# Optimization experiments

Measured on AMD Instinct MI355X. Metric: run time of the kernel, lower is better.

Reference implementation:

```python
import jax, jax.numpy as jnp
import numpy as np

EMBED_DIM = 400
NUM_HEADS = 4
HEAD_SIZE = EMBED_DIM // NUM_HEADS  # 100


def setup_inputs() -> dict:
    key = jax.random.key(0)
    ks = jax.random.split(key, 6)
    B, T = 8, 2048
    x = jax.random.normal(ks[0], (B, T, EMBED_DIM), dtype=jnp.float32)
    # per-head projection weights, stacked over heads: [H, C, D]
    scale = 1.0 / np.sqrt(EMBED_DIM)
    Wq = jax.random.normal(ks[1], (NUM_HEADS, EMBED_DIM, HEAD_SIZE), dtype=jnp.float32) * scale
    Wk = jax.random.normal(ks[2], (NUM_HEADS, EMBED_DIM, HEAD_SIZE), dtype=jnp.float32) * scale
    Wv = jax.random.normal(ks[3], (NUM_HEADS, EMBED_DIM, HEAD_SIZE), dtype=jnp.float32) * scale
    Wo = jax.random.normal(ks[4], (EMBED_DIM, EMBED_DIM), dtype=jnp.float32) * scale
    bo = jax.random.normal(ks[5], (EMBED_DIM,), dtype=jnp.float32) * scale
    return {"x": x, "Wq": Wq, "Wk": Wk, "Wv": Wv, "Wo": Wo, "bo": bo}


def reference(x, Wq, Wk, Wv, Wo, bo):
    B, T, C = x.shape
    inv_sqrt_d = 1.0 / jnp.sqrt(jnp.asarray(HEAD_SIZE, x.dtype))
    # project: [B,T,C] x [H,C,D] -> [B,H,T,D]
    q = jnp.einsum('btc,hcd->bhtd', x, Wq)
    k = jnp.einsum('btc,hcd->bhtd', x, Wk)
    v = jnp.einsum('btc,hcd->bhtd', x, Wv)
    scores = jnp.einsum('bhtd,bhsd->bhts', q, k) * inv_sqrt_d  # [B,H,T,T]
    causal = jnp.tril(jnp.ones((T, T), dtype=bool))
    scores = jnp.where(causal, scores, -jnp.inf)
    attn = jax.nn.softmax(scores, axis=-1)
    out = jnp.einsum('bhts,bhsd->bhtd', attn, v)  # [B,H,T,D]
    # concat heads (head order matches torch concat on last dim)
    out = out.transpose(0, 2, 1, 3).reshape(B, T, C)
    # output projection; dropout is identity in eval mode
    return out @ Wo.T + bo
```

## Files before the change

kernel.cpp:

```cpp
#include <hip/hip_runtime.h>
#include <hip/hip_bf16.h>

#define B_ 8
#define T_ 2048
#define C_ 400
#define H_ 4
#define D_ 100
#define DP 128
#define KP 416
#define KPB 832

typedef __hip_bfloat16 bf16;
typedef unsigned int uint32;
typedef __attribute__((ext_vector_type(8))) short short8;
typedef __attribute__((ext_vector_type(4))) float f32x4;

__device__ __forceinline__ float bf2f(bf16 v){ return __bfloat162float(v); }
__device__ __forceinline__ bf16 f2bf(float f){ return __float2bfloat16(f); }
__device__ __forceinline__ unsigned short bfbits(float f){
  bf16 h = f2bf(f);
  return __builtin_bit_cast(unsigned short, h);
}
__device__ __forceinline__ uint32 pk2(float a, float b){
  return (uint32)bfbits(a) | ((uint32)bfbits(b) << 16);
}
__device__ __forceinline__ void gl_lds16(const char* gsrc, char* ldst){
  __builtin_amdgcn_global_load_lds(
      (const __attribute__((address_space(1))) unsigned int*)gsrc,
      (__attribute__((address_space(3))) unsigned int*)ldst, 16, 0, 0);
}

__global__ __launch_bounds__(256) void conv_x_kernel(const float* __restrict__ x,
    bf16* __restrict__ xb){
  int i = blockIdx.x*256 + threadIdx.x;
  if (i >= 16384*52) return;
  int c8 = i % 52, t = i / 52;
  uint32 u[4];
  if (c8 < 50){
    const float* src = x + (size_t)t*C_ + c8*8;
    #pragma unroll
    for (int k=0;k<4;++k) u[k] = pk2(src[2*k], src[2*k+1]);
  } else {
    u[0]=u[1]=u[2]=u[3]=0;
  }
  *reinterpret_cast<uint4*>((char*)xb + (size_t)t*KPB + c8*16) = make_uint4(u[0],u[1],u[2],u[3]);
}

__global__ __launch_bounds__(256) void prep_wqkv_kernel(const float* __restrict__ Wq,
    const float* __restrict__ Wk, const float* __restrict__ Wv, bf16* __restrict__ WT){
  int i = blockIdx.x*256 + threadIdx.x;
  if (i >= 12*128*KP) return;
  int c = i % KP, n = (i/KP) & 127, group = i/(KP*128);
  int p = group >> 2, h = group & 3;
  float v = 0.f;
  if (n < D_ && c < C_){
    const float* W = (p==0)?Wq:(p==1)?Wk:Wv;
    v = W[((size_t)h*C_ + c)*D_ + n];
  }
  WT[i] = f2bf(v);
}

__global__ __launch_bounds__(256) void prep_wo_kernel(const float* __restrict__ Wo,
    bf16* __restrict__ WoB){
  int i = blockIdx.x*256 + threadIdx.x;
  if (i >= 512*KP) return;
  int c = i % KP, n = i / KP;
  float v = (n < C_ && c < C_) ? Wo[(size_t)n*C_ + c] : 0.f;
  WoB[i] = f2bf(v);
}

__global__ __launch_bounds__(256) void zero_aopad_kernel(bf16* __restrict__ AOb){
  int i = blockIdx.x*256 + threadIdx.x;
  if (i >= 16384*2) return;
  int row = i >> 1, half = i & 1;
  *reinterpret_cast<uint4*>((char*)AOb + (size_t)row*KPB + 800 + half*16) = make_uint4(0,0,0,0);
}

__global__ __launch_bounds__(256) void qkv_gemm_kernel(const bf16* __restrict__ xb,
    const bf16* __restrict__ WT, bf16* __restrict__ Qp, bf16* __restrict__ Kp,
    bf16* __restrict__ VT){
  __shared__ __align__(16) char xs[2][8192];
  __shared__ __align__(16) char wsh[2][8192];
  int bid = blockIdx.x;
  int xcd = bid & 7, idx = bid >> 3;
  int mb = xcd*16 + idx/12;
  int group = idx % 12;
  int p = group >> 2, h = group & 3;
  int t0 = mb * 128;
  int tid = threadIdx.x;
  int w = tid >> 6, l = tid & 63, g = l >> 4, qi = l & 15;
  const char* xg = (const char*)xb + (size_t)t0*KPB;
  const char* wg = (const char*)WT + (size_t)group*128*KPB;
  int srow = tid >> 2, sseg = tid & 3;

  #define GSTAGE(J, BUF) {                                                     \
    int kc2 = (J)*64;                                                          \
    _Pragma("unroll")                                                          \
    for (int r2=0;r2<2;++r2)                                                   \
      gl_lds16(xg + (size_t)(srow + r2*64)*KPB + kc2 + sseg*16,                \
               &xs[BUF][tid*16 + r2*4096]);                                    \
    _Pragma("unroll")                                                          \
    for (int r2=0;r2<2;++r2)                                                   \
      gl_lds16(wg + (size_t)(srow + r2*64)*KPB + kc2 + sseg*16,                \
               &wsh[BUF][tid*16 + r2*4096]); }

  f32x4 acc[2][8];
  #pragma unroll
  for (int mt=0;mt<2;++mt)
    #pragma unroll
    for (int nt=0;nt<8;++nt) acc[mt][nt] = (f32x4){0.f,0.f,0.f,0.f};

  GSTAGE(0, 0)
  __syncthreads();
  for (int j = 0; j < 13; ++j){
    int cur = j & 1;
    if (j < 12) GSTAGE(j+1, cur^1)
    short8 af[2];
    #pragma unroll
    for (int mt=0;mt<2;++mt)
      af[mt] = *reinterpret_cast<const short8*>(&xs[cur][(w*32 + mt*16 + qi)*64 + g*16]);
    short8 bfr[8];
    #pragma unroll
    for (int nt=0;nt<8;++nt)
      bfr[nt] = *reinterpret_cast<const short8*>(&wsh[cur][(nt*16 + qi)*64 + g*16]);
    if (p < 2){
      #pragma unroll
      for (int mt=0;mt<2;++mt)
        #pragma unroll
        for (int nt=0;nt<8;++nt)
          acc[mt][nt] = __builtin_amdgcn_mfma_f32_16x16x32_bf16(af[mt], bfr[nt], acc[mt][nt], 0,0,0);
    } else {
      #pragma unroll
      for (int mt=0;mt<2;++mt)
        #pragma unroll
        for (int nt=0;nt<8;++nt)
          acc[mt][nt] = __builtin_amdgcn_mfma_f32_16x16x32_bf16(bfr[nt], af[mt], acc[mt][nt], 0,0,0);
    }
    __syncthreads();
  }

  int b = t0 >> 11, tloc0 = t0 & 2047;
  size_t bh = (size_t)b*H_ + h;
  if (p < 2){
    bf16* dst = (p==0 ? Qp : Kp) + (bh*T_ + tloc0)*DP;
    #pragma unroll
    for (int mt=0;mt<2;++mt)
      #pragma unroll
      for (int r=0;r<4;++r){
        int tr = w*32 + mt*16 + 4*g + r;
        #pragma unroll
        for (int nt=0;nt<8;++nt)
          dst[(size_t)tr*DP + nt*16 + qi] = f2bf(acc[mt][nt][r]);
      }
  } else {
    bf16* dstv = VT + bh*DP*T_ + tloc0;
    #pragma unroll
    for (int nt=0;nt<8;++nt)
      #pragma unroll
      for (int r=0;r<4;++r){
        int d = nt*16 + 4*g + r;
        #pragma unroll
        for (int mt=0;mt<2;++mt)
          dstv[(size_t)d*T_ + w*32 + mt*16 + qi] = f2bf(acc[mt][nt][r]);
      }
  }
  #undef GSTAGE
}

__global__ __launch_bounds__(256) void out_gemm_kernel(const bf16* __restrict__ AOb,
    const bf16* __restrict__ WoB, const float* __restrict__ bo, float* __restrict__ out){
  __shared__ __align__(16) char xs[2][8192];
  __shared__ __align__(16) char wsh[2][8192];
  int bid = blockIdx.x;
  int xcd = bid & 7, idx = bid >> 3;
  int mb = xcd*16 + idx/4;
  int nb = idx & 3;
  int t0 = mb * 128, n0 = nb * 128;
  int tid = threadIdx.x;
  int w = tid >> 6, l = tid & 63, g = l >> 4, qi = l & 15;
  const char* xg = (const char*)AOb + (size_t)t0*KPB;
  const char* wg = (const char*)WoB + (size_t)n0*KPB;
  int srow = tid >> 2, sseg = tid & 3;

  #define GSTAGE(J, BUF) {                                                     \
    int kc2 = (J)*64;                                                          \
    _Pragma("unroll")                                                          \
    for (int r2=0;r2<2;++r2)                                                   \
      gl_lds16(xg + (size_t)(srow + r2*64)*KPB + kc2 + sseg*16,                \
               &xs[BUF][tid*16 + r2*4096]);                                    \
    _Pragma("unroll")                                                          \
    for (int r2=0;r2<2;++r2)                                                   \
      gl_lds16(wg + (size_t)(srow + r2*64)*KPB + kc2 + sseg*16,                \
               &wsh[BUF][tid*16 + r2*4096]); }

  f32x4 acc[2][8];
  #pragma unroll
  for (int mt=0;mt<2;++mt)
    #pragma unroll
    for (int nt=0;nt<8;++nt) acc[mt][nt] = (f32x4){0.f,0.f,0.f,0.f};

  GSTAGE(0, 0)
  __syncthreads();
  for (int j = 0; j < 13; ++j){
    int cur = j & 1;
    if (j < 12) GSTAGE(j+1, cur^1)
    short8 af[2];
    #pragma unroll
    for (int mt=0;mt<2;++mt)
      af[mt] = *reinterpret_cast<const short8*>(&xs[cur][(w*32 + mt*16 + qi)*64 + g*16]);
    short8 bfr[8];
    #pragma unroll
    for (int nt=0;nt<8;++nt)
      bfr[nt] = *reinterpret_cast<const short8*>(&wsh[cur][(nt*16 + qi)*64 + g*16]);
    #pragma unroll
    for (int mt=0;mt<2;++mt)
      #pragma unroll
      for (int nt=0;nt<8;++nt)
        acc[mt][nt] = __builtin_amdgcn_mfma_f32_16x16x32_bf16(af[mt], bfr[nt], acc[mt][nt], 0,0,0);
    __syncthreads();
  }

  #pragma unroll
  for (int nt=0;nt<8;++nt){
    if (n0 + nt*16 >= C_) continue;
    int n = n0 + nt*16 + qi;
    float bv = bo[n];
    #pragma unroll
    for (int mt=0;mt<2;++mt)
      #pragma unroll
      for (int r=0;r<4;++r){
        int tr = w*32 + mt*16 + 4*g + r;
        out[(size_t)(t0 + tr)*C_ + n] = acc[mt][nt][r] + bv;
      }
  }
  #undef GSTAGE
}

__global__ __launch_bounds__(256) void attn_kernel(const bf16* __restrict__ Qp,
    const bf16* __restrict__ Kp, const bf16* __restrict__ VT, bf16* __restrict__ AOb){
  __shared__ __align__(16) char ktile[2][16384];
  __shared__ __align__(16) char vtile[2][14336];
  __shared__ __align__(16) uint32 pshare[4*16*36];
  const float NEGINF = -__builtin_inff();
  int bid = blockIdx.x;
  int xcd = bid & 7, idx = bid >> 3;
  int bh  = xcd*4 + (idx >> 5);
  int qb  = 31 - (idx & 31);
  int tid = threadIdx.x;
  int w = tid >> 6, l = tid & 63;
  int g = l >> 4, qi = l & 15;
  int q0 = qb*64 + w*16;

  const bf16* Qrow  = Qp + ((size_t)bh*T_ + q0 + qi)*DP + g*8;
  const char* Kg    = (const char*)(Kp + (size_t)bh*T_*DP);
  const char* Vg    = (const char*)(VT + (size_t)bh*DP*T_);

  short8 qf[4];
  #pragma unroll
  for (int ks=0; ks<4; ++ks)
    qf[ks] = *reinterpret_cast<const short8*>(Qrow + ks*32);

  f32x4 acc[7];
  #pragma unroll
  for (int dt=0; dt<7; ++dt) acc[dt] = (f32x4){0.f,0.f,0.f,0.f};
  float m = NEGINF, lr = 0.f;

  uint32* pbase = &pshare[(w*16 + qi)*36];
  int qglob = q0 + qi;
  int nch = qb + 1;

  int st_off0 = w*4096 + l*16;
  #define STAGE(J, BUF) { int k0s = (J) << 6;                                   \
    _Pragma("unroll")                                                           \
    for (int it=0; it<4; ++it){                                                 \
      int off = st_off0 + it*1024;                                              \
      int row = off >> 8;                                                       \
      int cb  = off & 255;                                                      \
      gl_lds16(Kg + (size_t)(k0s + row)*256 + (cb ^ ((row&15)<<4)),             \
               &ktile[BUF][w*4096 + it*1024]); } }

  #define VSTAGE(J, BUF) { int k0s2 = ((J) << 6)*2;                             \
    for (int it=w; it<14; it+=4){                                               \
      int off = it*1024 + l*16;                                                 \
      int row = off >> 7;                                                       \
      int cb  = off & 127;                                                      \
      gl_lds16(Vg + (size_t)row*(T_*2) + k0s2 + (cb ^ ((row&7)<<4)),            \
               &vtile[BUF][it*1024 + l*16]); } }

  STAGE(0, 0)
  VSTAGE(0, 0)
  __syncthreads();

  for (int j = 0; j < nch; ++j){
    int k0 = j << 6;
    int cur = j & 1;
    if (j + 1 < nch){ STAGE(j+1, cur^1) VSTAGE(j+1, cur^1) }
    const char* kb = ktile[cur];
    const char* vb = vtile[cur];
    f32x4 st[4];
    __builtin_amdgcn_s_setprio(1);
    #pragma unroll
    for (int kt=0; kt<4; ++kt){
      f32x4 s = (f32x4){0.f,0.f,0.f,0.f};
      #pragma unroll
      for (int ks=0; ks<4; ++ks){
        short8 kf = *reinterpret_cast<const short8*>(
            kb + (kt*16 + qi)*256 + ((ks*64 + g*16) ^ (qi<<4)));
        s = __builtin_amdgcn_mfma_f32_16x16x32_bf16(kf, qf[ks], s, 0, 0, 0);
      }
      st[kt] = s;
    }
    __builtin_amdgcn_s_setprio(0);
    float p[4][4];
    float cmax = NEGINF;
    if (j == nch - 1){
      #pragma unroll
      for (int kt=0; kt<4; ++kt)
        #pragma unroll
        for (int r=0; r<4; ++r){
          int key = k0 + kt*16 + 4*g + r;
          float v = st[kt][r]*0.1f; if (key > qglob) v = NEGINF;
          p[kt][r] = v; cmax = fmaxf(cmax, v);
        }
    } else {
      #pragma unroll
      for (int kt=0; kt<4; ++kt)
        #pragma unroll
        for (int r=0; r<4; ++r){
          float v = st[kt][r]*0.1f;
          p[kt][r] = v; cmax = fmaxf(cmax, v);
        }
    }
    cmax = fmaxf(cmax, __shfl_xor(cmax, 16));
    cmax = fmaxf(cmax, __shfl_xor(cmax, 32));
    float mnew = fmaxf(m, cmax);
    float scale = __expf(m - mnew);
    m = mnew;
    float rs = 0.f;
    #pragma unroll
    for (int kt=0; kt<4; ++kt)
      #pragma unroll
      for (int r=0; r<4; ++r){
        p[kt][r] = __expf(p[kt][r] - m);
        rs += p[kt][r];
      }
    rs += __shfl_xor(rs, 16);
    rs += __shfl_xor(rs, 32);
    lr = lr*scale + rs;
    float scr[4];
    #pragma unroll
    for (int r=0; r<4; ++r) scr[r] = __shfl(scale, 20*g + r);
    #pragma unroll
    for (int dt=0; dt<7; ++dt){
      acc[dt][0]*=scr[0]; acc[dt][1]*=scr[1]; acc[dt][2]*=scr[2]; acc[dt][3]*=scr[3];
    }
    #pragma unroll
    for (int kt=0; kt<4; ++kt){
      pbase[kt*8 + 2*g    ] = pk2(p[kt][0], p[kt][1]);
      pbase[kt*8 + 2*g + 1] = pk2(p[kt][2], p[kt][3]);
    }
    __builtin_amdgcn_s_setprio(1);
    #pragma unroll
    for (int ks=0; ks<2; ++ks){
      short8 pa = *reinterpret_cast<const short8*>(pbase + 16*ks + 4*g);
      #pragma unroll
      for (int dt=0; dt<7; ++dt){
        int row = dt*16 + qi;
        short8 vf = *reinterpret_cast<const short8*>(
            vb + row*128 + ((ks*64 + g*16) ^ ((qi&7)<<4)));
        acc[dt] = __builtin_amdgcn_mfma_f32_16x16x32_bf16(pa, vf, acc[dt], 0, 0, 0);
      }
    }
    __builtin_amdgcn_s_setprio(0);
    __syncthreads();
  }
  float inv = 1.f / lr;
  float invr[4];
  #pragma unroll
  for (int r=0; r<4; ++r) invr[r] = __shfl(inv, 20*g + r);
  int b = bh >> 2, h = bh & 3;
  #pragma unroll
  for (int dt=0; dt<7; ++dt){
    int d = dt*16 + qi;
    if (d < D_){
      #pragma unroll
      for (int r=0; r<4; ++r){
        size_t row = (size_t)(b*T_) + q0 + 4*g + r;
        AOb[row*KP + h*D_ + d] = f2bf(acc[dt][r] * invr[r]);
      }
    }
  }
  #undef STAGE
  #undef VSTAGE
}

extern "C" void kernel_launch(void* const* d_in, const int* in_sizes, int n_in,
                              void* d_out, int out_size, void* d_ws, size_t ws_size,
                              hipStream_t stream){
  const float* x  = (const float*)d_in[0];
  const float* Wq = (const float*)d_in[1];
  const float* Wk = (const float*)d_in[2];
  const float* Wv = (const float*)d_in[3];
  const float* Wo = (const float*)d_in[4];
  const float* bo = (const float*)d_in[5];

  constexpr size_t NBH  = (size_t)B_*H_;
  constexpr size_t NPAD = NBH*T_*DP;
  constexpr size_t NROW = (size_t)B_*T_;
  constexpr size_t OFF_QP  = 0;
  constexpr size_t OFF_KP  = OFF_QP + NPAD*2;
  constexpr size_t OFF_VT  = OFF_KP + NPAD*2;
  constexpr size_t OFF_XB  = OFF_VT + NPAD*2;
  constexpr size_t OFF_AOB = OFF_XB + NROW*KP*2;
  constexpr size_t OFF_WT  = OFF_AOB + NROW*KP*2;
  constexpr size_t OFF_WOB = OFF_WT + (size_t)12*128*KP*2;
  constexpr size_t TOTAL   = OFF_WOB + (size_t)512*KP*2;
  if (ws_size < TOTAL) return;

  char* ws = (char*)d_ws;
  bf16*  Qp   = (bf16*)(ws + OFF_QP);
  bf16*  Kp   = (bf16*)(ws + OFF_KP);
  bf16*  VTp  = (bf16*)(ws + OFF_VT);
  bf16*  xb   = (bf16*)(ws + OFF_XB);
  bf16*  AOb  = (bf16*)(ws + OFF_AOB);
  bf16*  WT   = (bf16*)(ws + OFF_WT);
  bf16*  WoB  = (bf16*)(ws + OFF_WOB);
  float* out  = (float*)d_out;

  conv_x_kernel<<<(16384*52 + 255)/256, 256, 0, stream>>>(x, xb);
  prep_wqkv_kernel<<<(12*128*KP + 255)/256, 256, 0, stream>>>(Wq, Wk, Wv, WT);
  prep_wo_kernel<<<(512*KP + 255)/256, 256, 0, stream>>>(Wo, WoB);
  zero_aopad_kernel<<<128, 256, 0, stream>>>(AOb);
  qkv_gemm_kernel<<<1536, 256, 0, stream>>>(xb, WT, Qp, Kp, VTp);
  attn_kernel<<<NBH*32, 256, 0, stream>>>(Qp, Kp, VTp, AOb);
  out_gemm_kernel<<<512, 256, 0, stream>>>(AOb, WoB, bo, out);
}
```

Baseline: 166.4 us.

## Double attention query tile per block, fold softmax scale into Q, lazy rescale

Each attention block now processes 128 queries (two 16-row query tiles per wave) instead of 64, so every staged K/V tile in LDS is reused across twice as many queries and the grid shrinks to 512 blocks. The 1/sqrt(d)*log2(e) factor is folded into Q at projection time so the softmax uses exp2 without a per-score multiply. Rescaling of the running output is skipped unless the row max grows by more than a threshold. Chunks lying entirely above the causal diagonal for a wave are skipped. The cost is more registers per thread (launch bounds set to 2 blocks), fewer blocks for load balancing across the causal triangle, and a small bf16 rounding change from scaling Q before conversion.

```diff
diff --git a/kernel.cpp b/kernel.cpp
--- a/kernel.cpp
+++ b/kernel.cpp
@@ -9,6 +9,7 @@
 #define DP 128
 #define KP 416
 #define KPB 832
+#define QSCALE 0.14426950408889634f
 
 typedef __hip_bfloat16 bf16;
 typedef unsigned int uint32;
@@ -142,6 +143,7 @@
   int b = t0 >> 11, tloc0 = t0 & 2047;
   size_t bh = (size_t)b*H_ + h;
   if (p < 2){
+    float qs = (p==0) ? QSCALE : 1.0f;
     bf16* dst = (p==0 ? Qp : Kp) + (bh*T_ + tloc0)*DP;
     #pragma unroll
     for (int mt=0;mt<2;++mt)
@@ -150,7 +152,7 @@
         int tr = w*32 + mt*16 + 4*g + r;
         #pragma unroll
         for (int nt=0;nt<8;++nt)
-          dst[(size_t)tr*DP + nt*16 + qi] = f2bf(acc[mt][nt][r]);
+          dst[(size_t)tr*DP + nt*16 + qi] = f2bf(qs * acc[mt][nt][r]);
       }
   } else {
     bf16* dstv = VT + bh*DP*T_ + tloc0;
@@ -236,38 +238,40 @@
   #undef GSTAGE
 }
 
-__global__ __launch_bounds__(256) void attn_kernel(const bf16* __restrict__ Qp,
+__global__ __launch_bounds__(256, 2) void attn_kernel(const bf16* __restrict__ Qp,
     const bf16* __restrict__ Kp, const bf16* __restrict__ VT, bf16* __restrict__ AOb){
   __shared__ __align__(16) char ktile[2][16384];
   __shared__ __align__(16) char vtile[2][14336];
-  __shared__ __align__(16) uint32 pshare[4*16*36];
+  __shared__ __align__(16) uint32 pshare[4*2*16*36];
   const float NEGINF = -__builtin_inff();
   int bid = blockIdx.x;
   int xcd = bid & 7, idx = bid >> 3;
-  int bh  = xcd*4 + (idx >> 5);
-  int qb  = 31 - (idx & 31);
+  int bh  = xcd*4 + (idx >> 4);
+  int qb  = 15 - (idx & 15);
   int tid = threadIdx.x;
   int w = tid >> 6, l = tid & 63;
   int g = l >> 4, qi = l & 15;
-  int q0 = qb*64 + w*16;
+  int q0 = qb*128 + w*32;
 
   const bf16* Qrow  = Qp + ((size_t)bh*T_ + q0 + qi)*DP + g*8;
   const char* Kg    = (const char*)(Kp + (size_t)bh*T_*DP);
   const char* Vg    = (const char*)(VT + (size_t)bh*DP*T_);
 
-  short8 qf[4];
-  #pragma unroll
-  for (int ks=0; ks<4; ++ks)
-    qf[ks] = *reinterpret_cast<const short8*>(Qrow + ks*32);
-
-  f32x4 acc[7];
-  #pragma unroll
-  for (int dt=0; dt<7; ++dt) acc[dt] = (f32x4){0.f,0.f,0.f,0.f};
-  float m = NEGINF, lr = 0.f;
-
-  uint32* pbase = &pshare[(w*16 + qi)*36];
-  int qglob = q0 + qi;
-  int nch = qb + 1;
+  short8 qf[2][4];
+  #pragma unroll
+  for (int qt=0; qt<2; ++qt)
+    #pragma unroll
+    for (int ks=0; ks<4; ++ks)
+      qf[qt][ks] = *reinterpret_cast<const short8*>(Qrow + qt*16*DP + ks*32);
+
+  f32x4 acc[2][7];
+  #pragma unroll
+  for (int qt=0; qt<2; ++qt)
+    #pragma unroll
+    for (int dt=0; dt<7; ++dt) acc[qt][dt] = (f32x4){0.f,0.f,0.f,0.f};
+  float m[2] = {NEGINF, NEGINF}, lr[2] = {0.f, 0.f};
+
+  int nch = 2*qb + 2;
 
   int st_off0 = w*4096 + l*16;
   #define STAGE(J, BUF) { int k0s = (J) << 6;                                   \
@@ -295,98 +299,113 @@
     int k0 = j << 6;
     int cur = j & 1;
     if (j + 1 < nch){ STAGE(j+1, cur^1) VSTAGE(j+1, cur^1) }
-    const char* kb = ktile[cur];
-    const char* vb = vtile[cur];
-    f32x4 st[4];
-    __builtin_amdgcn_s_setprio(1);
-    #pragma unroll
-    for (int kt=0; kt<4; ++kt){
-      f32x4 s = (f32x4){0.f,0.f,0.f,0.f};
-      #pragma unroll
-      for (int ks=0; ks<4; ++ks){
-        short8 kf = *reinterpret_cast<const short8*>(
-            kb + (kt*16 + qi)*256 + ((ks*64 + g*16) ^ (qi<<4)));
-        s = __builtin_amdgcn_mfma_f32_16x16x32_bf16(kf, qf[ks], s, 0, 0, 0);
-      }
-      st[kt] = s;
-    }
-    __builtin_amdgcn_s_setprio(0);
-    float p[4][4];
-    float cmax = NEGINF;
-    if (j == nch - 1){
-      #pragma unroll
-      for (int kt=0; kt<4; ++kt)
-        #pragma unroll
-        for (int r=0; r<4; ++r){
-          int key = k0 + kt*16 + 4*g + r;
-          float v = st[kt][r]*0.1f; if (key > qglob) v = NEGINF;
-          p[kt][r] = v; cmax = fmaxf(cmax, v);
-        }
-    } else {
-      #pragma unroll
-      for (int kt=0; kt<4; ++kt)
-        #pragma unroll
-        for (int r=0; r<4; ++r){
-          float v = st[kt][r]*0.1f;
-          p[kt][r] = v; cmax = fmaxf(cmax, v);
-        }
-    }
-    cmax = fmaxf(cmax, __shfl_xor(cmax, 16));
-    cmax = fmaxf(cmax, __shfl_xor(cmax, 32));
-    float mnew = fmaxf(m, cmax);
-    float scale = __expf(m - mnew);
-    m = mnew;
-    float rs = 0.f;
-    #pragma unroll
-    for (int kt=0; kt<4; ++kt)
-      #pragma unroll
-      for (int r=0; r<4; ++r){
-        p[kt][r] = __expf(p[kt][r] - m);
-        rs += p[kt][r];
-      }
-    rs += __shfl_xor(rs, 16);
-    rs += __shfl_xor(rs, 32);
-    lr = lr*scale + rs;
-    float scr[4];
-    #pragma unroll
-    for (int r=0; r<4; ++r) scr[r] = __shfl(scale, 20*g + r);
-    #pragma unroll
-    for (int dt=0; dt<7; ++dt){
-      acc[dt][0]*=scr[0]; acc[dt][1]*=scr[1]; acc[dt][2]*=scr[2]; acc[dt][3]*=scr[3];
-    }
-    #pragma unroll
-    for (int kt=0; kt<4; ++kt){
-      pbase[kt*8 + 2*g    ] = pk2(p[kt][0], p[kt][1]);
-      pbase[kt*8 + 2*g + 1] = pk2(p[kt][2], p[kt][3]);
-    }
-    __builtin_amdgcn_s_setprio(1);
-    #pragma unroll
-    for (int ks=0; ks<2; ++ks){
-      short8 pa = *reinterpret_cast<const short8*>(pbase + 16*ks + 4*g);
-      #pragma unroll
-      for (int dt=0; dt<7; ++dt){
-        int row = dt*16 + qi;
-        short8 vf = *reinterpret_cast<const short8*>(
-            vb + row*128 + ((ks*64 + g*16) ^ ((qi&7)<<4)));
-        acc[dt] = __builtin_amdgcn_mfma_f32_16x16x32_bf16(pa, vf, acc[dt], 0, 0, 0);
+    if (k0 <= q0 + 31){
+      const char* kb = ktile[cur];
+      const char* vb = vtile[cur];
+      bool lastm = (k0 + 63 > q0);
+      #pragma unroll
+      for (int qt=0; qt<2; ++qt){
+        int qglob = q0 + qt*16 + qi;
+        f32x4 st[4];
+        __builtin_amdgcn_s_setprio(1);
+        #pragma unroll
+        for (int kt=0; kt<4; ++kt){
+          f32x4 s = (f32x4){0.f,0.f,0.f,0.f};
+          #pragma unroll
+          for (int ks=0; ks<4; ++ks){
+            short8 kf = *reinterpret_cast<const short8*>(
+                kb + (kt*16 + qi)*256 + ((ks*64 + g*16) ^ (qi<<4)));
+            s = __builtin_amdgcn_mfma_f32_16x16x32_bf16(kf, qf[qt][ks], s, 0, 0, 0);
+          }
+          st[kt] = s;
+        }
+        __builtin_amdgcn_s_setprio(0);
+        float p[4][4];
+        float cmax = NEGINF;
+        if (lastm){
+          #pragma unroll
+          for (int kt=0; kt<4; ++kt)
+            #pragma unroll
+            for (int r=0; r<4; ++r){
+              int key = k0 + kt*16 + 4*g + r;
+              float v = st[kt][r]; if (key > qglob) v = NEGINF;
+              p[kt][r] = v; cmax = fmaxf(cmax, v);
+            }
+        } else {
+          #pragma unroll
+          for (int kt=0; kt<4; ++kt)
+            #pragma unroll
+            for (int r=0; r<4; ++r){
+              float v = st[kt][r];
+              p[kt][r] = v; cmax = fmaxf(cmax, v);
+            }
+        }
+        cmax = fmaxf(cmax, __shfl_xor(cmax, 16));
+        cmax = fmaxf(cmax, __shfl_xor(cmax, 32));
+        if (!__all(cmax - m[qt] <= 8.0f)){
+          float mnew = fmaxf(m[qt], cmax);
+          float scale = exp2f(m[qt] - mnew);
+          m[qt] = mnew;
+          lr[qt] *= scale;
+          float scr[4];
+          #pragma unroll
+          for (int r=0; r<4; ++r) scr[r] = __shfl(scale, 20*g + r);
+          #pragma unroll
+          for (int dt=0; dt<7; ++dt){
+            acc[qt][dt][0]*=scr[0]; acc[qt][dt][1]*=scr[1];
+            acc[qt][dt][2]*=scr[2]; acc[qt][dt][3]*=scr[3];
+          }
+        }
+        float rs = 0.f;
+        #pragma unroll
+        for (int kt=0; kt<4; ++kt)
+          #pragma unroll
+          for (int r=0; r<4; ++r){
+            p[kt][r] = exp2f(p[kt][r] - m[qt]);
+            rs += p[kt][r];
+          }
+        rs += __shfl_xor(rs, 16);
+        rs += __shfl_xor(rs, 32);
+        lr[qt] += rs;
+        uint32* pbase = &pshare[((w*2 + qt)*16 + qi)*36];
+        #pragma unroll
+        for (int kt=0; kt<4; ++kt){
+          pbase[kt*8 + 2*g    ] = pk2(p[kt][0], p[kt][1]);
+          pbase[kt*8 + 2*g + 1] = pk2(p[kt][2], p[kt][3]);
+        }
+        __builtin_amdgcn_s_setprio(1);
+        #pragma unroll
+        for (int ks=0; ks<2; ++ks){
+          short8 pa = *reinterpret_cast<const short8*>(pbase + 16*ks + 4*g);
+          #pragma unroll
+          for (int dt=0; dt<7; ++dt){
+            int row = dt*16 + qi;
+            short8 vf = *reinterpret_cast<const short8*>(
+                vb + row*128 + ((ks*64 + g*16) ^ ((qi&7)<<4)));
+            acc[qt][dt] = __builtin_amdgcn_mfma_f32_16x16x32_bf16(pa, vf, acc[qt][dt], 0, 0, 0);
+          }
+        }
+        __builtin_amdgcn_s_setprio(0);
       }
     }
-    __builtin_amdgcn_s_setprio(0);
     __syncthreads();
   }
-  float inv = 1.f / lr;
-  float invr[4];
-  #pragma unroll
-  for (int r=0; r<4; ++r) invr[r] = __shfl(inv, 20*g + r);
   int b = bh >> 2, h = bh & 3;
   #pragma unroll
-  for (int dt=0; dt<7; ++dt){
-    int d = dt*16 + qi;
-    if (d < D_){
-      #pragma unroll
-      for (int r=0; r<4; ++r){
-        size_t row = (size_t)(b*T_) + q0 + 4*g + r;
-        AOb[row*KP + h*D_ + d] = f2bf(acc[dt][r] * invr[r]);
+  for (int qt=0; qt<2; ++qt){
+    float inv = 1.f / lr[qt];
+    float invr[4];
+    #pragma unroll
+    for (int r=0; r<4; ++r) invr[r] = __shfl(inv, 20*g + r);
+    #pragma unroll
+    for (int dt=0; dt<7; ++dt){
+      int d = dt*16 + qi;
+      if (d < D_){
+        #pragma unroll
+        for (int r=0; r<4; ++r){
+          size_t row = (size_t)(b*T_) + q0 + qt*16 + 4*g + r;
+          AOb[row*KP + h*D_ + d] = f2bf(acc[qt][dt][r] * invr[r]);
+        }
       }
     }
   }
@@ -432,6 +451,6 @@
   prep_wo_kernel<<<(512*KP + 255)/256, 256, 0, stream>>>(Wo, WoB);
   zero_aopad_kernel<<<128, 256, 0, stream>>>(AOb);
   qkv_gemm_kernel<<<1536, 256, 0, stream>>>(xb, WT, Qp, Kp, VTp);
-  attn_kernel<<<NBH*32, 256, 0, stream>>>(Qp, Kp, VTp, AOb);
+  attn_kernel<<<512, 256, 0, stream>>>(Qp, Kp, VTp, AOb);
   out_gemm_kernel<<<512, 256, 0, stream>>>(AOb, WoB, bo, out);
 }
```

Result: slower. 178.3 us (+7.2%).

## Pair causal query blocks per workgroup and fold softmax scale into Q

Applied to the files above, without the earlier changes.

Each attention workgroup now processes two query blocks (qb and 31-qb) that share K/V tile loads, balancing causal work across 512 blocks and reusing staged K/V for both. The softmax scale and log2(e) factor are folded into Q during the projection, so the kernel uses exp2f, and rescaling of the running max is skipped unless the max grows by more than 8. This raises register pressure (two sets of accumulators and Q fragments, launch bounds of 2 waves per SIMD) and adds branches for the dual path.

```diff
diff --git a/kernel.cpp b/kernel.cpp
--- a/kernel.cpp
+++ b/kernel.cpp
@@ -9,6 +9,7 @@
 #define DP 128
 #define KP 416
 #define KPB 832
+#define QSCALE 0.14426950408889634f
 
 typedef __hip_bfloat16 bf16;
 typedef unsigned int uint32;
@@ -142,6 +143,7 @@
   int b = t0 >> 11, tloc0 = t0 & 2047;
   size_t bh = (size_t)b*H_ + h;
   if (p < 2){
+    float qs = (p==0) ? QSCALE : 1.0f;
     bf16* dst = (p==0 ? Qp : Kp) + (bh*T_ + tloc0)*DP;
     #pragma unroll
     for (int mt=0;mt<2;++mt)
@@ -150,7 +152,7 @@
         int tr = w*32 + mt*16 + 4*g + r;
         #pragma unroll
         for (int nt=0;nt<8;++nt)
-          dst[(size_t)tr*DP + nt*16 + qi] = f2bf(acc[mt][nt][r]);
+          dst[(size_t)tr*DP + nt*16 + qi] = f2bf(qs * acc[mt][nt][r]);
       }
   } else {
     bf16* dstv = VT + bh*DP*T_ + tloc0;
@@ -236,38 +238,44 @@
   #undef GSTAGE
 }
 
-__global__ __launch_bounds__(256) void attn_kernel(const bf16* __restrict__ Qp,
+__global__ __launch_bounds__(256, 2) void attn_kernel(const bf16* __restrict__ Qp,
     const bf16* __restrict__ Kp, const bf16* __restrict__ VT, bf16* __restrict__ AOb){
   __shared__ __align__(16) char ktile[2][16384];
   __shared__ __align__(16) char vtile[2][14336];
-  __shared__ __align__(16) uint32 pshare[4*16*36];
+  __shared__ __align__(16) uint32 pshare[4*2*16*36];
   const float NEGINF = -__builtin_inff();
   int bid = blockIdx.x;
   int xcd = bid & 7, idx = bid >> 3;
-  int bh  = xcd*4 + (idx >> 5);
-  int qb  = 31 - (idx & 31);
+  int bh  = xcd*4 + (idx & 3);
+  int pr  = idx >> 2;
+  int qbA = pr, qbB = 31 - pr;
   int tid = threadIdx.x;
   int w = tid >> 6, l = tid & 63;
   int g = l >> 4, qi = l & 15;
-  int q0 = qb*64 + w*16;
-
-  const bf16* Qrow  = Qp + ((size_t)bh*T_ + q0 + qi)*DP + g*8;
+  int q0A = qbA*64 + w*16, q0B = qbB*64 + w*16;
+  int nchA = qbA + 1, nchB = qbB + 1;
+
+  const bf16* Qbase = Qp + (size_t)bh*T_*DP + g*8;
   const char* Kg    = (const char*)(Kp + (size_t)bh*T_*DP);
   const char* Vg    = (const char*)(VT + (size_t)bh*DP*T_);
 
-  short8 qf[4];
-  #pragma unroll
-  for (int ks=0; ks<4; ++ks)
-    qf[ks] = *reinterpret_cast<const short8*>(Qrow + ks*32);
-
-  f32x4 acc[7];
-  #pragma unroll
-  for (int dt=0; dt<7; ++dt) acc[dt] = (f32x4){0.f,0.f,0.f,0.f};
-  float m = NEGINF, lr = 0.f;
-
-  uint32* pbase = &pshare[(w*16 + qi)*36];
-  int qglob = q0 + qi;
-  int nch = qb + 1;
+  short8 qfA[4], qfB[4];
+  #pragma unroll
+  for (int ks=0; ks<4; ++ks){
+    qfA[ks] = *reinterpret_cast<const short8*>(Qbase + (size_t)(q0A + qi)*DP + ks*32);
+    qfB[ks] = *reinterpret_cast<const short8*>(Qbase + (size_t)(q0B + qi)*DP + ks*32);
+  }
+
+  f32x4 accA[7], accB[7];
+  #pragma unroll
+  for (int dt=0; dt<7; ++dt){
+    accA[dt] = (f32x4){0.f,0.f,0.f,0.f};
+    accB[dt] = (f32x4){0.f,0.f,0.f,0.f};
+  }
+  float mA = NEGINF, mB = NEGINF, lrA = 0.f, lrB = 0.f;
+
+  uint32* pbB = &pshare[((w*2 + 0)*16 + qi)*36];
+  uint32* pbA = &pshare[((w*2 + 1)*16 + qi)*36];
 
   int st_off0 = w*4096 + l*16;
   #define STAGE(J, BUF) { int k0s = (J) << 6;                                   \
@@ -287,106 +295,130 @@
       gl_lds16(Vg + (size_t)row*(T_*2) + k0s2 + (cb ^ ((row&7)<<4)),            \
                &vtile[BUF][it*1024 + l*16]); } }
 
+  auto softpack = [&](const f32x4 st[4], f32x4 acc[7], float& m, float& lr,
+                      int qglob, int k0, bool maskch, uint32* pb){
+    float p[4][4];
+    float cmax = NEGINF;
+    if (maskch){
+      #pragma unroll
+      for (int kt=0; kt<4; ++kt)
+        #pragma unroll
+        for (int r=0; r<4; ++r){
+          int key = k0 + kt*16 + 4*g + r;
+          float v = st[kt][r]; if (key > qglob) v = NEGINF;
+          p[kt][r] = v; cmax = fmaxf(cmax, v);
+        }
+    } else {
+      #pragma unroll
+      for (int kt=0; kt<4; ++kt)
+        #pragma unroll
+        for (int r=0; r<4; ++r){
+          float v = st[kt][r];
+          p[kt][r] = v; cmax = fmaxf(cmax, v);
+        }
+    }
+    cmax = fmaxf(cmax, __shfl_xor(cmax, 16));
+    cmax = fmaxf(cmax, __shfl_xor(cmax, 32));
+    if (!__all(cmax - m <= 8.0f)){
+      float mnew = fmaxf(m, cmax);
+      float scale = exp2f(m - mnew);
+      m = mnew;
+      lr *= scale;
+      float scr[4];
+      #pragma unroll
+      for (int r=0; r<4; ++r) scr[r] = __shfl(scale, 20*g + r);
+      #pragma unroll
+      for (int dt=0; dt<7; ++dt){
+        acc[dt][0]*=scr[0]; acc[dt][1]*=scr[1]; acc[dt][2]*=scr[2]; acc[dt][3]*=scr[3];
+      }
+    }
+    float rs = 0.f;
+    #pragma unroll
+    for (int kt=0; kt<4; ++kt)
+      #pragma unroll
+      for (int r=0; r<4; ++r){
+        p[kt][r] = exp2f(p[kt][r] - m);
+        rs += p[kt][r];
+      }
+    rs += __shfl_xor(rs, 16);
+    rs += __shfl_xor(rs, 32);
+    lr += rs;
+    #pragma unroll
+    for (int kt=0; kt<4; ++kt){
+      pb[kt*8 + 2*g    ] = pk2(p[kt][0], p[kt][1]);
+      pb[kt*8 + 2*g + 1] = pk2(p[kt][2], p[kt][3]);
+    }
+  };
+
   STAGE(0, 0)
   VSTAGE(0, 0)
   __syncthreads();
 
-  for (int j = 0; j < nch; ++j){
+  for (int j = 0; j < nchB; ++j){
     int k0 = j << 6;
     int cur = j & 1;
-    if (j + 1 < nch){ STAGE(j+1, cur^1) VSTAGE(j+1, cur^1) }
+    if (j + 1 < nchB){ STAGE(j+1, cur^1) VSTAGE(j+1, cur^1) }
     const char* kb = ktile[cur];
     const char* vb = vtile[cur];
-    f32x4 st[4];
+    bool dual = (j < nchA);
+    f32x4 stA[4], stB[4];
     __builtin_amdgcn_s_setprio(1);
     #pragma unroll
     for (int kt=0; kt<4; ++kt){
-      f32x4 s = (f32x4){0.f,0.f,0.f,0.f};
+      f32x4 sB = (f32x4){0.f,0.f,0.f,0.f};
+      f32x4 sA = (f32x4){0.f,0.f,0.f,0.f};
       #pragma unroll
       for (int ks=0; ks<4; ++ks){
         short8 kf = *reinterpret_cast<const short8*>(
             kb + (kt*16 + qi)*256 + ((ks*64 + g*16) ^ (qi<<4)));
-        s = __builtin_amdgcn_mfma_f32_16x16x32_bf16(kf, qf[ks], s, 0, 0, 0);
-      }
-      st[kt] = s;
+        sB = __builtin_amdgcn_mfma_f32_16x16x32_bf16(kf, qfB[ks], sB, 0, 0, 0);
+        if (dual)
+          sA = __builtin_amdgcn_mfma_f32_16x16x32_bf16(kf, qfA[ks], sA, 0, 0, 0);
+      }
+      stB[kt] = sB; stA[kt] = sA;
     }
     __builtin_amdgcn_s_setprio(0);
-    float p[4][4];
-    float cmax = NEGINF;
-    if (j == nch - 1){
-      #pragma unroll
-      for (int kt=0; kt<4; ++kt)
-        #pragma unroll
-        for (int r=0; r<4; ++r){
-          int key = k0 + kt*16 + 4*g + r;
-          float v = st[kt][r]*0.1f; if (key > qglob) v = NEGINF;
-          p[kt][r] = v; cmax = fmaxf(cmax, v);
-        }
-    } else {
-      #pragma unroll
-      for (int kt=0; kt<4; ++kt)
-        #pragma unroll
-        for (int r=0; r<4; ++r){
-          float v = st[kt][r]*0.1f;
-          p[kt][r] = v; cmax = fmaxf(cmax, v);
-        }
-    }
-    cmax = fmaxf(cmax, __shfl_xor(cmax, 16));
-    cmax = fmaxf(cmax, __shfl_xor(cmax, 32));
-    float mnew = fmaxf(m, cmax);
-    float scale = __expf(m - mnew);
-    m = mnew;
-    float rs = 0.f;
-    #pragma unroll
-    for (int kt=0; kt<4; ++kt)
-      #pragma unroll
-      for (int r=0; r<4; ++r){
-        p[kt][r] = __expf(p[kt][r] - m);
-        rs += p[kt][r];
-      }
-    rs += __shfl_xor(rs, 16);
-    rs += __shfl_xor(rs, 32);
-    lr = lr*scale + rs;
-    float scr[4];
-    #pragma unroll
-    for (int r=0; r<4; ++r) scr[r] = __shfl(scale, 20*g + r);
-    #pragma unroll
-    for (int dt=0; dt<7; ++dt){
-      acc[dt][0]*=scr[0]; acc[dt][1]*=scr[1]; acc[dt][2]*=scr[2]; acc[dt][3]*=scr[3];
-    }
-    #pragma unroll
-    for (int kt=0; kt<4; ++kt){
-      pbase[kt*8 + 2*g    ] = pk2(p[kt][0], p[kt][1]);
-      pbase[kt*8 + 2*g + 1] = pk2(p[kt][2], p[kt][3]);
-    }
+    softpack(stB, accB, mB, lrB, q0B + qi, k0, j == nchB - 1, pbB);
+    if (dual)
+      softpack(stA, accA, mA, lrA, q0A + qi, k0, j == nchA - 1, pbA);
     __builtin_amdgcn_s_setprio(1);
     #pragma unroll
     for (int ks=0; ks<2; ++ks){
-      short8 pa = *reinterpret_cast<const short8*>(pbase + 16*ks + 4*g);
+      short8 paB = *reinterpret_cast<const short8*>(pbB + 16*ks + 4*g);
+      short8 paA = *reinterpret_cast<const short8*>(pbA + 16*ks + 4*g);
       #pragma unroll
       for (int dt=0; dt<7; ++dt){
         int row = dt*16 + qi;
         short8 vf = *reinterpret_cast<const short8*>(
             vb + row*128 + ((ks*64 + g*16) ^ ((qi&7)<<4)));
-        acc[dt] = __builtin_amdgcn_mfma_f32_16x16x32_bf16(pa, vf, acc[dt], 0, 0, 0);
+        accB[dt] = __builtin_amdgcn_mfma_f32_16x16x32_bf16(paB, vf, accB[dt], 0, 0, 0);
+        if (dual)
+          accA[dt] = __builtin_amdgcn_mfma_f32_16x16x32_bf16(paA, vf, accA[dt], 0, 0, 0);
       }
     }
     __builtin_amdgcn_s_setprio(0);
     __syncthreads();
   }
-  float inv = 1.f / lr;
-  float invr[4];
-  #pragma unroll
-  for (int r=0; r<4; ++r) invr[r] = __shfl(inv, 20*g + r);
+
   int b = bh >> 2, h = bh & 3;
   #pragma unroll
-  for (int dt=0; dt<7; ++dt){
-    int d = dt*16 + qi;
-    if (d < D_){
-      #pragma unroll
-      for (int r=0; r<4; ++r){
-        size_t row = (size_t)(b*T_) + q0 + 4*g + r;
-        AOb[row*KP + h*D_ + d] = f2bf(acc[dt][r] * invr[r]);
+  for (int tix=0; tix<2; ++tix){
+    f32x4* acc = tix ? accA : accB;
+    float lr = tix ? lrA : lrB;
+    int q0 = tix ? q0A : q0B;
+    float inv = 1.f / lr;
+    float invr[4];
+    #pragma unroll
+    for (int r=0; r<4; ++r) invr[r] = __shfl(inv, 20*g + r);
+    #pragma unroll
+    for (int dt=0; dt<7; ++dt){
+      int d = dt*16 + qi;
+      if (d < D_){
+        #pragma unroll
+        for (int r=0; r<4; ++r){
+          size_t row = (size_t)(b*T_) + q0 + 4*g + r;
+          AOb[row*KP + h*D_ + d] = f2bf(acc[dt][r] * invr[r]);
+        }
       }
     }
   }
@@ -432,6 +464,6 @@
   prep_wo_kernel<<<(512*KP + 255)/256, 256, 0, stream>>>(Wo, WoB);
   zero_aopad_kernel<<<128, 256, 0, stream>>>(AOb);
   qkv_gemm_kernel<<<1536, 256, 0, stream>>>(xb, WT, Qp, Kp, VTp);
-  attn_kernel<<<NBH*32, 256, 0, stream>>>(Qp, Kp, VTp, AOb);
+  attn_kernel<<<512, 256, 0, stream>>>(Qp, Kp, VTp, AOb);
   out_gemm_kernel<<<512, 256, 0, stream>>>(AOb, WoB, bo, out);
 }
```

New measurement: 151.7 us. -8.8%, faster.
